# Optimization experiments

Measured on AMD Instinct MI355X. Metric: run time of the kernel, lower is better.

The kernel has to match this reference:

```python
import jax, jax.numpy as jnp
import numpy as np

SIG_T_TRAIN = 0.07
SIG_T_INFER = 0.07
EPS = 1e-12  # torch F.normalize eps


def _l2_normalize(x):
    # matches torch.nn.functional.normalize(x, dim=-1): x / max(||x||_2, eps)
    nrm = jnp.sqrt(jnp.sum(x * x, axis=-1, keepdims=True))
    return x / jnp.maximum(nrm, EPS)


def setup_inputs() -> dict:
    key = jax.random.key(0)
    k1, k2 = jax.random.split(key)
    v_feat = jax.random.normal(k1, (32, 16, 256, 512), dtype=jnp.float32)  # (b,n,t,d)
    t_feat = jax.random.normal(k2, (512, 512), dtype=jnp.float32)          # (c,d)
    return {"v_feat": v_feat, "t_feat": t_feat, "split": 1}


def reference(v_feat, t_feat, split):
    # split: 1 -> 'test' (normalize + sig_T_infer), 0 -> train (sig_T_train)
    if split == 1:
        tau = SIG_T_INFER
        v_feat = _l2_normalize(v_feat)
        t_feat = _l2_normalize(t_feat)
    else:
        tau = SIG_T_TRAIN
    # Original: dist = einsum('bntd,bmcd->bctnm', v, t_repeated)/tau, then mean over m, then n.
    # t_repeated is identical along m (a pure repeat), so mean over m is a no-op, and the
    # mean over n commutes with the linear contraction: reduce over n first, never
    # materializing the (b,c,t,n,m) tensor.
    v_mean = jnp.mean(v_feat, axis=1)  # (b,t,d)
    dist = jnp.einsum('btd,cd->bct', v_mean, t_feat) / tau  # (b,c,t)
    return dist
```

## Files before the change

kernel.cpp:

```cpp
#include <hip/hip_runtime.h>
#include <hip/hip_bf16.h>

typedef unsigned short u16;
typedef unsigned int u32;

typedef __bf16 bf16x8 __attribute__((ext_vector_type(8)));
typedef float f32x4 __attribute__((ext_vector_type(4)));

__device__ __forceinline__ u16 f2bf(float f) {
    u32 u = __float_as_uint(f);
    u32 r = (u + 0x7fffu + ((u >> 16) & 1u)) >> 16;
    return (u16)r;
}

__global__ void tnorm_kernel(const float* __restrict__ t_feat,
                             u16* __restrict__ tn,
                             const int* __restrict__ splitp) {
    const int row  = blockIdx.x;
    const int lane = threadIdx.x;
    const float* rp = t_feat + (size_t)row * 512 + lane * 8;
    float4 x0 = *reinterpret_cast<const float4*>(rp);
    float4 x1 = *reinterpret_cast<const float4*>(rp + 4);
    float s = x0.x*x0.x + x0.y*x0.y + x0.z*x0.z + x0.w*x0.w
            + x1.x*x1.x + x1.y*x1.y + x1.z*x1.z + x1.w*x1.w;
#pragma unroll
    for (int off = 32; off > 0; off >>= 1) s += __shfl_xor(s, off, 64);
    float inv = 1.0f;
    if (*splitp == 1) inv = 1.0f / fmaxf(sqrtf(s), 1e-12f);
    u32 p0 = (u32)f2bf(x0.x*inv) | ((u32)f2bf(x0.y*inv) << 16);
    u32 p1 = (u32)f2bf(x0.z*inv) | ((u32)f2bf(x0.w*inv) << 16);
    u32 p2 = (u32)f2bf(x1.x*inv) | ((u32)f2bf(x1.y*inv) << 16);
    u32 p3 = (u32)f2bf(x1.z*inv) | ((u32)f2bf(x1.w*inv) << 16);
    uint4 packed; packed.x = p0; packed.y = p1; packed.z = p2; packed.w = p3;
    reinterpret_cast<uint4*>(tn)[row * 64 + lane] = packed;
}

__global__ void vmean_kernel(const float* __restrict__ v,
                             u16* __restrict__ vm,
                             const int* __restrict__ splitp) {
    const int t    = blockIdx.x;
    const int b    = blockIdx.y;
    const int tid  = threadIdx.x;
    const int w    = tid >> 6;
    const int lane = tid & 63;
    const int split = *splitp;
    __shared__ float lds[4 * 512];

    float acc[8];
#pragma unroll
    for (int i = 0; i < 8; i++) acc[i] = 0.f;

#pragma unroll
    for (int nn = 0; nn < 4; nn++) {
        const int n = w + nn * 4;
        const float* row = v + ((((size_t)b * 16 + n) * 256 + t) * 512) + lane * 8;
        float4 x0 = *reinterpret_cast<const float4*>(row);
        float4 x1 = *reinterpret_cast<const float4*>(row + 4);
        float s = x0.x*x0.x + x0.y*x0.y + x0.z*x0.z + x0.w*x0.w
                + x1.x*x1.x + x1.y*x1.y + x1.z*x1.z + x1.w*x1.w;
#pragma unroll
        for (int off = 32; off > 0; off >>= 1) s += __shfl_xor(s, off, 64);
        float inv = 1.0f;
        if (split == 1) inv = 1.0f / fmaxf(sqrtf(s), 1e-12f);
        acc[0] += x0.x * inv; acc[1] += x0.y * inv;
        acc[2] += x0.z * inv; acc[3] += x0.w * inv;
        acc[4] += x1.x * inv; acc[5] += x1.y * inv;
        acc[6] += x1.z * inv; acc[7] += x1.w * inv;
    }
#pragma unroll
    for (int i = 0; i < 8; i += 2) {
        float2 p; p.x = acc[i]; p.y = acc[i + 1];
        *reinterpret_cast<float2*>(&lds[w * 512 + lane * 8 + i]) = p;
    }
    __syncthreads();
    float2 r; r.x = 0.f; r.y = 0.f;
#pragma unroll
    for (int w2 = 0; w2 < 4; w2++) {
        float2 p = *reinterpret_cast<const float2*>(&lds[w2 * 512 + tid * 2]);
        r.x += p.x; r.y += p.y;
    }
    r.x *= (1.0f / 16.0f); r.y *= (1.0f / 16.0f);
    u32 packed = (u32)f2bf(r.x) | ((u32)f2bf(r.y) << 16);
    reinterpret_cast<u32*>(vm)[(((size_t)b * 256 + t) << 8) + tid] = packed;
}

__global__ __launch_bounds__(256) void gemm_kernel(const u16* __restrict__ tn,
                                                   const u16* __restrict__ vm,
                                                   float* __restrict__ out) {
    const int bx   = blockIdx.x;
    const int by   = blockIdx.y;
    const int b    = blockIdx.z;
    const int tid  = threadIdx.x;
    const int lane = tid & 63;
    const int wid  = tid >> 6;
    const int wm   = wid & 1;
    const int wn   = wid >> 1;
    const int quad = lane >> 4;
    const int l15  = lane & 15;

    __shared__ u16 At[64 * 72];
    __shared__ u16 Bt[64 * 72];

    const int c0 = bx * 64, t0 = by * 64;
    f32x4 acc[2][2] = {};

    const int lrow = tid >> 3;
    const int lcol = (tid & 7) * 8;

    const uint4* gA = reinterpret_cast<const uint4*>(tn);
    const uint4* gB = reinterpret_cast<const uint4*>(vm) + (size_t)b * 256 * 64;

    for (int k0 = 0; k0 < 512; k0 += 64) {
#pragma unroll
        for (int it = 0; it < 2; it++) {
            int row = lrow + it * 32;
            uint4 av = gA[(c0 + row) * 64 + (k0 >> 3) + (tid & 7)];
            uint4 bv = gB[(t0 + row) * 64 + (k0 >> 3) + (tid & 7)];
            *reinterpret_cast<uint4*>(&At[row * 72 + lcol]) = av;
            *reinterpret_cast<uint4*>(&Bt[row * 72 + lcol]) = bv;
        }
        __syncthreads();
#pragma unroll
        for (int kk = 0; kk < 64; kk += 32) {
            bf16x8 af[2], bfr[2];
#pragma unroll
            for (int i = 0; i < 2; i++)
                af[i] = *reinterpret_cast<const bf16x8*>(
                    &At[(wm * 32 + i * 16 + l15) * 72 + kk + quad * 8]);
#pragma unroll
            for (int j = 0; j < 2; j++)
                bfr[j] = *reinterpret_cast<const bf16x8*>(
                    &Bt[(wn * 32 + j * 16 + l15) * 72 + kk + quad * 8]);
#pragma unroll
            for (int i = 0; i < 2; i++)
#pragma unroll
                for (int j = 0; j < 2; j++)
                    acc[i][j] = __builtin_amdgcn_mfma_f32_16x16x32_bf16(
                        af[i], bfr[j], acc[i][j], 0, 0, 0);
        }
        __syncthreads();
    }

    const float s = 1.0f / 0.07f;
    float* ob = out + (size_t)b * 131072;
#pragma unroll
    for (int i = 0; i < 2; i++)
#pragma unroll
        for (int j = 0; j < 2; j++)
#pragma unroll
            for (int r = 0; r < 4; r++) {
                int c = c0 + wm * 32 + i * 16 + quad * 4 + r;
                int t = t0 + wn * 32 + j * 16 + l15;
                ob[c * 256 + t] = acc[i][j][r] * s;
            }
}

extern "C" void kernel_launch(void* const* d_in, const int* in_sizes, int n_in,
                              void* d_out, int out_size, void* d_ws, size_t ws_size,
                              hipStream_t stream) {
    const float* v_feat = (const float*)d_in[0];
    const float* t_feat = (const float*)d_in[1];
    const int*   splitp = (const int*)d_in[2];
    float* out = (float*)d_out;

    u16* tn = (u16*)d_ws;
    u16* vm = tn + 512 * 512;

    tnorm_kernel<<<dim3(512), dim3(64), 0, stream>>>(t_feat, tn, splitp);
    vmean_kernel<<<dim3(256, 32), dim3(256), 0, stream>>>(v_feat, vm, splitp);
    gemm_kernel<<<dim3(8, 4, 32), dim3(256), 0, stream>>>(tn, vm, out);
}
```

Measured before the change: 371.8 us.

## Restructure GEMM to keep B fragments in registers and stream A directly

```diff
diff --git a/kernel.cpp b/kernel.cpp
--- a/kernel.cpp
+++ b/kernel.cpp
@@ -9,8 +9,7 @@
 
 __device__ __forceinline__ u16 f2bf(float f) {
     u32 u = __float_as_uint(f);
-    u32 r = (u + 0x7fffu + ((u >> 16) & 1u)) >> 16;
-    return (u16)r;
+    return (u16)((u + 0x7fffu + ((u >> 16) & 1u)) >> 16);
 }
 
 __global__ void tnorm_kernel(const float* __restrict__ t_feat,
@@ -87,72 +86,48 @@
 __global__ __launch_bounds__(256) void gemm_kernel(const u16* __restrict__ tn,
                                                    const u16* __restrict__ vm,
                                                    float* __restrict__ out) {
-    const int bx   = blockIdx.x;
-    const int by   = blockIdx.y;
-    const int b    = blockIdx.z;
+    const int tt   = blockIdx.x;
+    const int b    = blockIdx.y;
     const int tid  = threadIdx.x;
+    const int w    = tid >> 6;
     const int lane = tid & 63;
-    const int wid  = tid >> 6;
-    const int wm   = wid & 1;
-    const int wn   = wid >> 1;
     const int quad = lane >> 4;
     const int l15  = lane & 15;
+    const int t0   = tt * 16;
 
-    __shared__ u16 At[64 * 72];
-    __shared__ u16 Bt[64 * 72];
-
-    const int c0 = bx * 64, t0 = by * 64;
-    f32x4 acc[2][2] = {};
-
-    const int lrow = tid >> 3;
-    const int lcol = (tid & 7) * 8;
+    const uint4* gB = reinterpret_cast<const uint4*>(vm) + (size_t)b * 256 * 64;
+    bf16x8 breg[16];
+#pragma unroll
+    for (int kk = 0; kk < 16; ++kk) {
+        uint4 bv = gB[(t0 + l15) * 64 + kk * 4 + quad];
+        breg[kk] = *reinterpret_cast<const bf16x8*>(&bv);
+    }
 
     const uint4* gA = reinterpret_cast<const uint4*>(tn);
-    const uint4* gB = reinterpret_cast<const uint4*>(vm) + (size_t)b * 256 * 64;
+    const float sc = 1.0f / 0.07f;
+    float* ob = out + (size_t)b * (512 * 256);
 
-    for (int k0 = 0; k0 < 512; k0 += 64) {
+#pragma unroll 1
+    for (int f = 0; f < 8; f += 2) {
+        const int cb0 = w * 128 + f * 16;
+        const int cb1 = cb0 + 16;
+        f32x4 a0 = {};
+        f32x4 a1 = {};
+#pragma unroll 4
+        for (int kk = 0; kk < 16; ++kk) {
+            uint4 av0 = gA[(cb0 + l15) * 64 + kk * 4 + quad];
+            uint4 av1 = gA[(cb1 + l15) * 64 + kk * 4 + quad];
+            a0 = __builtin_amdgcn_mfma_f32_16x16x32_bf16(
+                *reinterpret_cast<const bf16x8*>(&av0), breg[kk], a0, 0, 0, 0);
+            a1 = __builtin_amdgcn_mfma_f32_16x16x32_bf16(
+                *reinterpret_cast<const bf16x8*>(&av1), breg[kk], a1, 0, 0, 0);
+        }
 #pragma unroll
-        for (int it = 0; it < 2; it++) {
-            int row = lrow + it * 32;
-            uint4 av = gA[(c0 + row) * 64 + (k0 >> 3) + (tid & 7)];
-            uint4 bv = gB[(t0 + row) * 64 + (k0 >> 3) + (tid & 7)];
-            *reinterpret_cast<uint4*>(&At[row * 72 + lcol]) = av;
-            *reinterpret_cast<uint4*>(&Bt[row * 72 + lcol]) = bv;
+        for (int r = 0; r < 4; ++r) {
+            ob[(cb0 + quad * 4 + r) * 256 + t0 + l15] = a0[r] * sc;
+            ob[(cb1 + quad * 4 + r) * 256 + t0 + l15] = a1[r] * sc;
         }
-        __syncthreads();
-#pragma unroll
-        for (int kk = 0; kk < 64; kk += 32) {
-            bf16x8 af[2], bfr[2];
-#pragma unroll
-            for (int i = 0; i < 2; i++)
-                af[i] = *reinterpret_cast<const bf16x8*>(
-                    &At[(wm * 32 + i * 16 + l15) * 72 + kk + quad * 8]);
-#pragma unroll
-            for (int j = 0; j < 2; j++)
-                bfr[j] = *reinterpret_cast<const bf16x8*>(
-                    &Bt[(wn * 32 + j * 16 + l15) * 72 + kk + quad * 8]);
-#pragma unroll
-            for (int i = 0; i < 2; i++)
-#pragma unroll
-                for (int j = 0; j < 2; j++)
-                    acc[i][j] = __builtin_amdgcn_mfma_f32_16x16x32_bf16(
-                        af[i], bfr[j], acc[i][j], 0, 0, 0);
-        }
-        __syncthreads();
     }
-
-    const float s = 1.0f / 0.07f;
-    float* ob = out + (size_t)b * 131072;
-#pragma unroll
-    for (int i = 0; i < 2; i++)
-#pragma unroll
-        for (int j = 0; j < 2; j++)
-#pragma unroll
-            for (int r = 0; r < 4; r++) {
-                int c = c0 + wm * 32 + i * 16 + quad * 4 + r;
-                int t = t0 + wn * 32 + j * 16 + l15;
-                ob[c * 256 + t] = acc[i][j][r] * s;
-            }
 }
 
 extern "C" void kernel_launch(void* const* d_in, const int* in_sizes, int n_in,
@@ -168,5 +143,5 @@
 
     tnorm_kernel<<<dim3(512), dim3(64), 0, stream>>>(t_feat, tn, splitp);
     vmean_kernel<<<dim3(256, 32), dim3(256), 0, stream>>>(v_feat, vm, splitp);
-    gemm_kernel<<<dim3(8, 4, 32), dim3(256), 0, stream>>>(tn, vm, out);
+    gemm_kernel<<<dim3(16, 32), dim3(256), 0, stream>>>(tn, vm, out);
 }
```

After: 417.5 us. 12.3% more time.

## Fold t-normalization into vmean launch and enlarge GEMM tile to 128x64

Applied to the files above, without the earlier changes.

```diff
diff --git a/kernel.cpp b/kernel.cpp
--- a/kernel.cpp
+++ b/kernel.cpp
@@ -9,41 +9,44 @@
 
 __device__ __forceinline__ u16 f2bf(float f) {
     u32 u = __float_as_uint(f);
-    u32 r = (u + 0x7fffu + ((u >> 16) & 1u)) >> 16;
-    return (u16)r;
-}
-
-__global__ void tnorm_kernel(const float* __restrict__ t_feat,
-                             u16* __restrict__ tn,
-                             const int* __restrict__ splitp) {
-    const int row  = blockIdx.x;
-    const int lane = threadIdx.x;
-    const float* rp = t_feat + (size_t)row * 512 + lane * 8;
-    float4 x0 = *reinterpret_cast<const float4*>(rp);
-    float4 x1 = *reinterpret_cast<const float4*>(rp + 4);
-    float s = x0.x*x0.x + x0.y*x0.y + x0.z*x0.z + x0.w*x0.w
-            + x1.x*x1.x + x1.y*x1.y + x1.z*x1.z + x1.w*x1.w;
-#pragma unroll
-    for (int off = 32; off > 0; off >>= 1) s += __shfl_xor(s, off, 64);
-    float inv = 1.0f;
-    if (*splitp == 1) inv = 1.0f / fmaxf(sqrtf(s), 1e-12f);
-    u32 p0 = (u32)f2bf(x0.x*inv) | ((u32)f2bf(x0.y*inv) << 16);
-    u32 p1 = (u32)f2bf(x0.z*inv) | ((u32)f2bf(x0.w*inv) << 16);
-    u32 p2 = (u32)f2bf(x1.x*inv) | ((u32)f2bf(x1.y*inv) << 16);
-    u32 p3 = (u32)f2bf(x1.z*inv) | ((u32)f2bf(x1.w*inv) << 16);
-    uint4 packed; packed.x = p0; packed.y = p1; packed.z = p2; packed.w = p3;
-    reinterpret_cast<uint4*>(tn)[row * 64 + lane] = packed;
+    return (u16)((u + 0x7fffu + ((u >> 16) & 1u)) >> 16);
 }
 
 __global__ void vmean_kernel(const float* __restrict__ v,
+                             const float* __restrict__ t_feat,
                              u16* __restrict__ vm,
+                             u16* __restrict__ tn,
                              const int* __restrict__ splitp) {
-    const int t    = blockIdx.x;
-    const int b    = blockIdx.y;
+    const int bx   = blockIdx.x;
+    const int by   = blockIdx.y;
     const int tid  = threadIdx.x;
     const int w    = tid >> 6;
     const int lane = tid & 63;
     const int split = *splitp;
+
+    if (by == 32) {
+        if (w >= 2) return;
+        const int row = bx * 2 + w;
+        const float* rp = t_feat + (size_t)row * 512 + lane * 8;
+        float4 x0 = *reinterpret_cast<const float4*>(rp);
+        float4 x1 = *reinterpret_cast<const float4*>(rp + 4);
+        float s = x0.x*x0.x + x0.y*x0.y + x0.z*x0.z + x0.w*x0.w
+                + x1.x*x1.x + x1.y*x1.y + x1.z*x1.z + x1.w*x1.w;
+#pragma unroll
+        for (int off = 32; off > 0; off >>= 1) s += __shfl_xor(s, off, 64);
+        float inv = 1.0f;
+        if (split == 1) inv = 1.0f / fmaxf(sqrtf(s), 1e-12f);
+        u32 p0 = (u32)f2bf(x0.x*inv) | ((u32)f2bf(x0.y*inv) << 16);
+        u32 p1 = (u32)f2bf(x0.z*inv) | ((u32)f2bf(x0.w*inv) << 16);
+        u32 p2 = (u32)f2bf(x1.x*inv) | ((u32)f2bf(x1.y*inv) << 16);
+        u32 p3 = (u32)f2bf(x1.z*inv) | ((u32)f2bf(x1.w*inv) << 16);
+        uint4 pk; pk.x = p0; pk.y = p1; pk.z = p2; pk.w = p3;
+        reinterpret_cast<uint4*>(tn)[row * 64 + lane] = pk;
+        return;
+    }
+
+    const int t = bx;
+    const int b = by;
     __shared__ float lds[4 * 512];
 
     float acc[8];
@@ -98,11 +101,11 @@
     const int quad = lane >> 4;
     const int l15  = lane & 15;
 
-    __shared__ u16 At[64 * 72];
+    __shared__ u16 At[128 * 72];
     __shared__ u16 Bt[64 * 72];
 
-    const int c0 = bx * 64, t0 = by * 64;
-    f32x4 acc[2][2] = {};
+    const int c0 = bx * 128, t0 = by * 64;
+    f32x4 acc[4][2] = {};
 
     const int lrow = tid >> 3;
     const int lcol = (tid & 7) * 8;
@@ -112,27 +115,31 @@
 
     for (int k0 = 0; k0 < 512; k0 += 64) {
 #pragma unroll
+        for (int it = 0; it < 4; it++) {
+            int row = lrow + it * 32;
+            uint4 av = gA[(c0 + row) * 64 + (k0 >> 3) + (tid & 7)];
+            *reinterpret_cast<uint4*>(&At[row * 72 + lcol]) = av;
+        }
+#pragma unroll
         for (int it = 0; it < 2; it++) {
             int row = lrow + it * 32;
-            uint4 av = gA[(c0 + row) * 64 + (k0 >> 3) + (tid & 7)];
             uint4 bv = gB[(t0 + row) * 64 + (k0 >> 3) + (tid & 7)];
-            *reinterpret_cast<uint4*>(&At[row * 72 + lcol]) = av;
             *reinterpret_cast<uint4*>(&Bt[row * 72 + lcol]) = bv;
         }
         __syncthreads();
 #pragma unroll
         for (int kk = 0; kk < 64; kk += 32) {
-            bf16x8 af[2], bfr[2];
+            bf16x8 af[4], bfr[2];
 #pragma unroll
-            for (int i = 0; i < 2; i++)
+            for (int i = 0; i < 4; i++)
                 af[i] = *reinterpret_cast<const bf16x8*>(
-                    &At[(wm * 32 + i * 16 + l15) * 72 + kk + quad * 8]);
+                    &At[(wm * 64 + i * 16 + l15) * 72 + kk + quad * 8]);
 #pragma unroll
             for (int j = 0; j < 2; j++)
                 bfr[j] = *reinterpret_cast<const bf16x8*>(
                     &Bt[(wn * 32 + j * 16 + l15) * 72 + kk + quad * 8]);
 #pragma unroll
-            for (int i = 0; i < 2; i++)
+            for (int i = 0; i < 4; i++)
 #pragma unroll
                 for (int j = 0; j < 2; j++)
                     acc[i][j] = __builtin_amdgcn_mfma_f32_16x16x32_bf16(
@@ -144,12 +151,12 @@
     const float s = 1.0f / 0.07f;
     float* ob = out + (size_t)b * 131072;
 #pragma unroll
-    for (int i = 0; i < 2; i++)
+    for (int i = 0; i < 4; i++)
 #pragma unroll
         for (int j = 0; j < 2; j++)
 #pragma unroll
             for (int r = 0; r < 4; r++) {
-                int c = c0 + wm * 32 + i * 16 + quad * 4 + r;
+                int c = c0 + wm * 64 + i * 16 + quad * 4 + r;
                 int t = t0 + wn * 32 + j * 16 + l15;
                 ob[c * 256 + t] = acc[i][j][r] * s;
             }
@@ -166,7 +173,6 @@
     u16* tn = (u16*)d_ws;
     u16* vm = tn + 512 * 512;
 
-    tnorm_kernel<<<dim3(512), dim3(64), 0, stream>>>(t_feat, tn, splitp);
-    vmean_kernel<<<dim3(256, 32), dim3(256), 0, stream>>>(v_feat, vm, splitp);
-    gemm_kernel<<<dim3(8, 4, 32), dim3(256), 0, stream>>>(tn, vm, out);
+    vmean_kernel<<<dim3(256, 33), dim3(256), 0, stream>>>(v_feat, t_feat, vm, tn, splitp);
+    gemm_kernel<<<dim3(4, 4, 32), dim3(256), 0, stream>>>(tn, vm, out);
 }
```

New measurement: 366.8 us. About the same (-1.3%).
